# Kernel optimization log

Hardware: AMD Instinct MI355X
Metric: run time of the kernel (lower is better)

## Reference

```python
import jax, jax.numpy as jnp
import numpy as np

D_MODEL = 512
HEADS = 8

def setup_inputs() -> dict:
    key = jax.random.key(0)
    ks = jax.random.split(key, 11)
    B, S, D = 2, 4096, D_MODEL
    s = 1.0 / np.sqrt(D)
    inp = {
        'q': jax.random.normal(ks[0], (B, S, D), jnp.float32),
        'k': jax.random.normal(ks[1], (B, S, D), jnp.float32),
        'v': jax.random.normal(ks[2], (B, S, D), jnp.float32),
        'Wq': jax.random.normal(ks[3], (D, D), jnp.float32) * s,
        'bq': jnp.zeros((D,), jnp.float32),
        'Wk': jax.random.normal(ks[4], (D, D), jnp.float32) * s,
        'bk': jnp.zeros((D,), jnp.float32),
        'Wv': jax.random.normal(ks[5], (D, D), jnp.float32) * s,
        'bv': jnp.zeros((D,), jnp.float32),
        'Wo': jax.random.normal(ks[6], (D, D), jnp.float32) * s,
        'bo': jnp.zeros((D,), jnp.float32),
    }
    return inp

def _split_heads(x, h):
    B, S, D = x.shape
    return x.reshape(B, S, h, D // h).transpose(0, 2, 1, 3)  # [B,H,S,Dh]

def reference(q, k, v, Wq, bq, Wk, bk, Wv, bv, Wo, bo):
    # torch Linear: y = x @ W.T + b
    qh = _split_heads(q @ Wq.T + bq, HEADS)
    kh = _split_heads(k @ Wk.T + bk, HEADS)
    vh = _split_heads(v @ Wv.T + bv, HEADS)
    d_tensor = qh.shape[-1]
    scale = 1.0 / jnp.sqrt(jnp.asarray(d_tensor, qh.dtype))
    score = jnp.einsum('bhqd,bhkd->bhqk', qh, kh) * scale  # [B,H,S,S]
    attn = jax.nn.softmax(score, axis=-1)
    out = jnp.einsum('bhqk,bhkd->bhqd', attn, vh)
    B, H, S, Dh = out.shape
    out = out.transpose(0, 2, 1, 3).reshape(B, S, H * Dh)
    return out @ Wo.T + bo
```

## Files before the change

kernel.cpp:

```cpp
#include <hip/hip_runtime.h>

typedef short bf16x8 __attribute__((ext_vector_type(8)));
typedef float f32x2 __attribute__((ext_vector_type(2)));
typedef float f32x4 __attribute__((ext_vector_type(4)));
typedef float f32x16 __attribute__((ext_vector_type(16)));
typedef unsigned short ushort_t;
typedef unsigned short us8 __attribute__((ext_vector_type(8)));
typedef unsigned short us4 __attribute__((ext_vector_type(4)));
typedef unsigned int u32x4 __attribute__((ext_vector_type(4)));
typedef unsigned int uint2v __attribute__((ext_vector_type(2)));

#define MFMA16(a, b, c) __builtin_amdgcn_mfma_f32_16x16x32_bf16((a), (b), (c), 0, 0, 0)
#define MFMA32(a, b, c) __builtin_amdgcn_mfma_f32_32x32x16_bf16((a), (b), (c), 0, 0, 0)

template <int N> struct ic { static constexpr int value = N; };

static __device__ __forceinline__ ushort_t f2bf(float f) {
    unsigned int u = __builtin_bit_cast(unsigned int, f);
    u += 0x7FFFu + ((u >> 16) & 1u);
    return (ushort_t)(u >> 16);
}

static __device__ __forceinline__ unsigned cvtpk(float lo, float hi) {
    unsigned r;
    asm("v_cvt_pk_bf16_f32 %0, %1, %2" : "=v"(r) : "v"(lo), "v"(hi));
    return r;
}

static __device__ __forceinline__ void gload16(const void* g, void* l) {
    __builtin_amdgcn_global_load_lds(
        (const __attribute__((address_space(1))) unsigned int*)g,
        (__attribute__((address_space(3))) unsigned int*)l,
        16, 0, 0);
}

__global__ __launch_bounds__(256) void cvt_w(const float* __restrict__ W0,
                                             const float* __restrict__ W1,
                                             const float* __restrict__ W2,
                                             const float* __restrict__ W3,
                                             ushort_t* __restrict__ dst) {
    const float* src = (blockIdx.y == 0) ? W0 : (blockIdx.y == 1) ? W1
                     : (blockIdx.y == 2) ? W2 : W3;
    const int i = (blockIdx.x * 256 + threadIdx.x) * 8;
    float4 f0 = *(const float4*)(src + i);
    float4 f1 = *(const float4*)(src + i + 4);
    unsigned tw[4] = {cvtpk(f0.x, f0.y), cvtpk(f0.z, f0.w),
                      cvtpk(f1.x, f1.y), cvtpk(f1.z, f1.w)};
    *(u32x4*)(dst + (size_t)blockIdx.y * 262144 + i) = *(u32x4*)tw;
}

__global__ __launch_bounds__(256) void gemm_qkv(const float* __restrict__ qi,
                                                const float* __restrict__ ki,
                                                const float* __restrict__ vi,
                                                const ushort_t* __restrict__ Wball,
                                                const float* __restrict__ bq,
                                                const float* __restrict__ bk,
                                                const float* __restrict__ bv,
                                                ushort_t* __restrict__ Qh,
                                                ushort_t* __restrict__ Kh,
                                                ushort_t* __restrict__ Vt,
                                                float Cs) {
    constexpr int K = 512;
    __shared__ ushort_t As[64][72];
    __shared__ ushort_t Bs[64][72];

    const int which = blockIdx.y;
    const float*    Ap   = (which == 0) ? qi : (which == 1) ? ki : vi;
    const ushort_t* Wb   = Wball + (size_t)which * 262144;
    const float*    bias = (which == 0) ? bq : (which == 1) ? bk : bv;
    ushort_t*       outp = (which == 0) ? Qh : (which == 1) ? Kh : Vt;

    int bid = blockIdx.x;
    bid = (bid & 7) * 128 + (bid >> 3);
    const int bm = bid >> 3;
    const int bn = bid & 7;
    const int m0 = bm * 64, n0 = bn * 64;
    const int t    = threadIdx.x;
    const int lane = t & 63;
    const int wv   = t >> 6;
    const int wm   = wv >> 1, wn = wv & 1;
    const int lrow = t >> 2;
    const int lcol = (t & 3) * 16;

    const int l15 = lane & 15;
    const int l16 = lane >> 4;

    f32x4 acc[2][2] = {};

    const float*    apf = Ap + (size_t)(m0 + lrow) * K + lcol;
    const ushort_t* bpb = Wb + (size_t)(n0 + lrow) * K + lcol;

    us8 br0, br1;
    f32x4 af[4];

    af[0] = *(const f32x4*)apf;       af[1] = *(const f32x4*)(apf + 4);
    af[2] = *(const f32x4*)(apf + 8); af[3] = *(const f32x4*)(apf + 12);
    br0 = *(const us8*)bpb; br1 = *(const us8*)(bpb + 8);

#pragma unroll 1
    for (int kt = 0; kt < K / 64; ++kt) {
        __syncthreads();
        {
            unsigned tw[8];
#pragma unroll
            for (int i = 0; i < 4; ++i) {
                tw[2 * i]     = cvtpk(af[i][0], af[i][1]);
                tw[2 * i + 1] = cvtpk(af[i][2], af[i][3]);
            }
            *(u32x4*)&As[lrow][lcol]     = *(u32x4*)tw;
            *(u32x4*)&As[lrow][lcol + 8] = *(u32x4*)(tw + 4);
        }
        *(us8*)&Bs[lrow][lcol]     = br0;
        *(us8*)&Bs[lrow][lcol + 8] = br1;
        __syncthreads();

        if (kt < K / 64 - 1) {
            const int off = (kt + 1) * 64;
            const float* s = apf + off;
            af[0] = *(const f32x4*)s;       af[1] = *(const f32x4*)(s + 4);
            af[2] = *(const f32x4*)(s + 8); af[3] = *(const f32x4*)(s + 12);
            br0 = *(const us8*)(bpb + off); br1 = *(const us8*)(bpb + off + 8);
        }

#pragma unroll
        for (int kk = 0; kk < 2; ++kk) {
            bf16x8 a0 = *(const bf16x8*)&As[wm * 32 + l15][kk * 32 + l16 * 8];
            bf16x8 a1 = *(const bf16x8*)&As[wm * 32 + 16 + l15][kk * 32 + l16 * 8];
            bf16x8 b0 = *(const bf16x8*)&Bs[wn * 32 + l15][kk * 32 + l16 * 8];
            bf16x8 b1 = *(const bf16x8*)&Bs[wn * 32 + 16 + l15][kk * 32 + l16 * 8];
            acc[0][0] = MFMA16(a0, b0, acc[0][0]);
            acc[0][1] = MFMA16(a0, b1, acc[0][1]);
            acc[1][0] = MFMA16(a1, b0, acc[1][0]);
            acc[1][1] = MFMA16(a1, b1, acc[1][1]);
        }
    }

#pragma unroll
    for (int i = 0; i < 2; ++i)
#pragma unroll
        for (int j = 0; j < 2; ++j) {
            const int n  = n0 + wn * 32 + j * 16 + l15;
            const float bv_ = bias[n];
            const int h = n >> 6, d = n & 63;
            if (which == 2) {
                const int mbase = m0 + wm * 32 + i * 16 + l16 * 4;
                const int b = mbase >> 12, key = mbase & 4095;
                const int keyr = key & 63;
                const int ks = keyr >> 4, hc = (keyr >> 3) & 1, e0 = keyr & 7;
                const int db = d >> 5, dr = d & 31;
                ushort_t tmp[4];
#pragma unroll
                for (int v = 0; v < 4; ++v) tmp[v] = f2bf(acc[i][j][v] + bv_);
                *(us4*)(outp + (size_t)(b * 8 + h) * 262144 +
                        (size_t)(key >> 6) * 4096 +
                        db * 2048 + ks * 512 + (hc * 32 + dr) * 8 + e0) = *(us4*)tmp;
            } else if (which == 1) {
                const int jd = d >> 4, hc = (d >> 3) & 1, e = d & 7;
#pragma unroll
                for (int v = 0; v < 4; ++v) {
                    const int m = m0 + wm * 32 + i * 16 + l16 * 4 + v;
                    const int b = m >> 12, s = m & 4095;
                    const int r = s & 63, kb2 = r >> 5, kr = r & 31;
                    outp[(size_t)(b * 8 + h) * 262144 + (size_t)(s >> 6) * 4096 +
                         kb2 * 2048 + jd * 512 + (hc * 32 + kr) * 8 + e] =
                        f2bf(acc[i][j][v] + bv_);
                }
            } else {
#pragma unroll
                for (int v = 0; v < 4; ++v) {
                    const int m = m0 + wm * 32 + i * 16 + l16 * 4 + v;
                    const int b = m >> 12, s = m & 4095;
                    outp[(((size_t)(b * 8 + h)) * 4096 + s) * 64 + d] =
                        f2bf((acc[i][j][v] + bv_) * Cs);
                }
            }
        }
}

__global__ __launch_bounds__(256) void gemm_out(const ushort_t* __restrict__ Ap,
                                                const ushort_t* __restrict__ Wb,
                                                const float* __restrict__ bias,
                                                float* __restrict__ outp) {
    constexpr int K = 512;
    __shared__ ushort_t As[64][72];
    __shared__ ushort_t Bs[64][72];

    int bid = blockIdx.x;
    bid = (bid & 7) * 128 + (bid >> 3);
    const int bm = bid >> 3;
    const int bn = bid & 7;
    const int m0 = bm * 64, n0 = bn * 64;
    const int t    = threadIdx.x;
    const int lane = t & 63;
    const int wv   = t >> 6;
    const int wm   = wv >> 1, wn = wv & 1;
    const int lrow = t >> 2;
    const int lcol = (t & 3) * 16;

    const int l15 = lane & 15;
    const int l16 = lane >> 4;

    f32x4 acc[2][2] = {};

    const ushort_t* apb = Ap + (size_t)(m0 + lrow) * K + lcol;
    const ushort_t* bpb = Wb + (size_t)(n0 + lrow) * K + lcol;

    us8 ar0, ar1, br0, br1;
    ar0 = *(const us8*)apb; ar1 = *(const us8*)(apb + 8);
    br0 = *(const us8*)bpb; br1 = *(const us8*)(bpb + 8);

#pragma unroll 1
    for (int kt = 0; kt < K / 64; ++kt) {
        __syncthreads();
        *(us8*)&As[lrow][lcol]     = ar0;
        *(us8*)&As[lrow][lcol + 8] = ar1;
        *(us8*)&Bs[lrow][lcol]     = br0;
        *(us8*)&Bs[lrow][lcol + 8] = br1;
        __syncthreads();

        if (kt < K / 64 - 1) {
            const int off = (kt + 1) * 64;
            ar0 = *(const us8*)(apb + off); ar1 = *(const us8*)(apb + off + 8);
            br0 = *(const us8*)(bpb + off); br1 = *(const us8*)(bpb + off + 8);
        }

#pragma unroll
        for (int kk = 0; kk < 2; ++kk) {
            bf16x8 a0 = *(const bf16x8*)&As[wm * 32 + l15][kk * 32 + l16 * 8];
            bf16x8 a1 = *(const bf16x8*)&As[wm * 32 + 16 + l15][kk * 32 + l16 * 8];
            bf16x8 b0 = *(const bf16x8*)&Bs[wn * 32 + l15][kk * 32 + l16 * 8];
            bf16x8 b1 = *(const bf16x8*)&Bs[wn * 32 + 16 + l15][kk * 32 + l16 * 8];
            acc[0][0] = MFMA16(a0, b0, acc[0][0]);
            acc[0][1] = MFMA16(a0, b1, acc[0][1]);
            acc[1][0] = MFMA16(a1, b0, acc[1][0]);
            acc[1][1] = MFMA16(a1, b1, acc[1][1]);
        }
    }

#pragma unroll
    for (int i = 0; i < 2; ++i)
#pragma unroll
        for (int j = 0; j < 2; ++j) {
            const int n  = n0 + wn * 32 + j * 16 + l15;
            const float bv_ = bias[n];
#pragma unroll
            for (int v = 0; v < 4; ++v) {
                const int m = m0 + wm * 32 + i * 16 + l16 * 4 + v;
                outp[(size_t)m * 512 + n] = acc[i][j][v] + bv_;
            }
        }
}

__global__ __launch_bounds__(256) void attn_fwd(const ushort_t* __restrict__ Qh,
                                                const ushort_t* __restrict__ Kg,
                                                const ushort_t* __restrict__ Vg,
                                                ushort_t* __restrict__ Out) {
    constexpr int S  = 4096;
    constexpr int NT = 64;
    __shared__ __attribute__((aligned(16))) char LDS[32768];

    const int qt = blockIdx.x;
    const int bh = blockIdx.y;
    const int b  = bh >> 3, h = bh & 7;

    const int t    = threadIdx.x;
    const int lane = t & 63;
    const int wv   = t >> 6;
    const int l31  = lane & 31;
    const int hl   = lane >> 5;

    const int qw = qt * 128 + wv * 32;

    bf16x8 qf[4];
    {
        const ushort_t* qp = Qh + ((size_t)bh * S + qw + l31) * 64 + hl * 8;
#pragma unroll
        for (int ds = 0; ds < 4; ++ds) qf[ds] = *(const bf16x8*)(qp + ds * 16);
    }

    const f32x16 fzero = {};
    f32x16 accO[2] = {};
    float ll = 0.f;

    const char* lbase = LDS + lane * 16;
    const int wvb = wv * 1024;
    const ushort_t* kg = Kg + (size_t)bh * 262144 + wv * 512 + lane * 8;
    const ushort_t* vg = Vg + (size_t)bh * 262144 + wv * 512 + lane * 8;

    auto issue = [&](int kt, auto curc) {
        constexpr int CUR = decltype(curc)::value;
        const ushort_t* kg_ = kg + (size_t)kt * 4096;
        const ushort_t* vg_ = vg + (size_t)kt * 4096;
        gload16(kg_,        LDS + CUR * 8192 + wvb);
        gload16(kg_ + 2048, LDS + CUR * 8192 + 4096 + wvb);
        gload16(vg_,        LDS + 16384 + CUR * 8192 + wvb);
        gload16(vg_ + 2048, LDS + 16384 + CUR * 8192 + 4096 + wvb);
    };

    auto tile = [&](int kt, auto curc) {
        constexpr int CUR = decltype(curc)::value;

        f32x16 sc0, sc1;
        __builtin_amdgcn_s_setprio(1);
        {
            bf16x8 kf = *(const bf16x8*)(lbase + CUR * 8192);
            sc0 = MFMA32(kf, qf[0], fzero);
        }
#pragma unroll
        for (int ds = 1; ds < 4; ++ds) {
            bf16x8 kf = *(const bf16x8*)(lbase + CUR * 8192 + ds * 1024);
            sc0 = MFMA32(kf, qf[ds], sc0);
        }
        {
            bf16x8 kf = *(const bf16x8*)(lbase + CUR * 8192 + 4096);
            sc1 = MFMA32(kf, qf[0], fzero);
        }
#pragma unroll
        for (int ds = 1; ds < 4; ++ds) {
            bf16x8 kf = *(const bf16x8*)(lbase + CUR * 8192 + 4096 + ds * 1024);
            sc1 = MFMA32(kf, qf[ds], sc1);
        }
        __builtin_amdgcn_s_setprio(0);

#pragma unroll
        for (int i = 0; i < 16; ++i) {
            sc0[i] = __builtin_amdgcn_exp2f(sc0[i]);
            sc1[i] = __builtin_amdgcn_exp2f(sc1[i]);
        }

        {
#define PAIR(v, i) __builtin_shufflevector((v), (v), 2 * (i), 2 * (i) + 1)
            f32x2 pa = (PAIR(sc0, 0) + PAIR(sc0, 1)) + (PAIR(sc0, 2) + PAIR(sc0, 3));
            f32x2 pbt = (PAIR(sc0, 4) + PAIR(sc0, 5)) + (PAIR(sc0, 6) + PAIR(sc0, 7));
            f32x2 pc = (PAIR(sc1, 0) + PAIR(sc1, 1)) + (PAIR(sc1, 2) + PAIR(sc1, 3));
            f32x2 pd = (PAIR(sc1, 4) + PAIR(sc1, 5)) + (PAIR(sc1, 6) + PAIR(sc1, 7));
            f32x2 s2 = (pa + pbt) + (pc + pd);
            ll += s2.x + s2.y;
#undef PAIR
        }

        bf16x8 pb[4];
#pragma unroll
        for (int ks = 0; ks < 4; ++ks) {
            const int R0 = (ks & 1) * 8;
            float e0, e1, e2, e3, e4, e5, e6, e7;
            if (ks < 2) {
                e0 = sc0[R0+0]; e1 = sc0[R0+1]; e2 = sc0[R0+2]; e3 = sc0[R0+3];
                e4 = sc0[R0+4]; e5 = sc0[R0+5]; e6 = sc0[R0+6]; e7 = sc0[R0+7];
            } else {
                e0 = sc1[R0+0]; e1 = sc1[R0+1]; e2 = sc1[R0+2]; e3 = sc1[R0+3];
                e4 = sc1[R0+4]; e5 = sc1[R0+5]; e6 = sc1[R0+6]; e7 = sc1[R0+7];
            }
            unsigned w0 = cvtpk(e0, e1);
            unsigned w1 = cvtpk(e2, e3);
            unsigned w2 = cvtpk(e4, e5);
            unsigned w3 = cvtpk(e6, e7);
            uint2v s02 = __builtin_amdgcn_permlane32_swap(w0, w2, false, false);
            uint2v s13 = __builtin_amdgcn_permlane32_swap(w1, w3, false, false);
            u32x4 w = {s02.x, s13.x, s02.y, s13.y};
            pb[ks] = __builtin_bit_cast(bf16x8, w);
        }

        __builtin_amdgcn_s_setprio(1);
#pragma unroll
        for (int ks = 0; ks < 4; ++ks) {
            {
                bf16x8 vf = *(const bf16x8*)(lbase + 16384 + CUR * 8192 + ks * 1024);
                accO[0] = MFMA32(vf, pb[ks], accO[0]);
            }
            {
                bf16x8 vf = *(const bf16x8*)(lbase + 16384 + CUR * 8192 + 4096 + ks * 1024);
                accO[1] = MFMA32(vf, pb[ks], accO[1]);
            }
        }
        __builtin_amdgcn_s_setprio(0);

        __syncthreads();
        if (kt + 2 < NT) issue(kt + 2, curc);
    };

    issue(0, ic<0>{});
    issue(1, ic<1>{});
    __syncthreads();

#pragma unroll 1
    for (int kt2 = 0; kt2 < NT; kt2 += 2) {
        tile(kt2,     ic<0>{});
        tile(kt2 + 1, ic<1>{});
    }

    const float lt  = ll + __shfl_xor(ll, 32);
    const float inv = 1.0f / lt;
    ushort_t* orow = Out + ((size_t)b * S + qw + l31) * 512 + h * 64;
#pragma unroll
    for (int db = 0; db < 2; ++db)
#pragma unroll
        for (int q4 = 0; q4 < 4; ++q4) {
            unsigned w0 = cvtpk(accO[db][q4 * 4 + 0] * inv, accO[db][q4 * 4 + 1] * inv);
            unsigned w1 = cvtpk(accO[db][q4 * 4 + 2] * inv, accO[db][q4 * 4 + 3] * inv);
            unsigned tmp[2] = {w0, w1};
            *(us4*)(orow + db * 32 + q4 * 8 + hl * 4) = *(const us4*)tmp;
        }
}

extern "C" void kernel_launch(void* const* d_in, const int* in_sizes, int n_in,
                              void* d_out, int out_size, void* d_ws, size_t ws_size,
                              hipStream_t stream) {
    const float* q  = (const float*)d_in[0];
    const float* k  = (const float*)d_in[1];
    const float* v  = (const float*)d_in[2];
    const float* Wq = (const float*)d_in[3];
    const float* bq = (const float*)d_in[4];
    const float* bk = (const float*)d_in[6];
    const float* bv = (const float*)d_in[8];
    const float* bo = (const float*)d_in[10];

    char* w = (char*)d_ws;
    const size_t SZ = (size_t)2 * 8 * 4096 * 64 * 2;

    ushort_t* Qh  = (ushort_t*)(w);
    ushort_t* Kh  = (ushort_t*)(w + SZ);
    ushort_t* Vtr = (ushort_t*)(w + 2 * SZ);
    ushort_t* AO  = (ushort_t*)(w + 3 * SZ);
    ushort_t* Wb  = (ushort_t*)(w + 4 * SZ);

    cvt_w<<<dim3(128, 4), 256, 0, stream>>>(Wq, (const float*)d_in[5],
                                            (const float*)d_in[7], (const float*)d_in[9], Wb);

    const float Cs = 0.125f * 1.44269504f;
    gemm_qkv<<<dim3(1024, 3), 256, 0, stream>>>(q, k, v, Wb, bq, bk, bv, Qh, Kh, Vtr, Cs);

    attn_fwd<<<dim3(32, 16), 256, 0, stream>>>(Qh, Kh, Vtr, AO);

    gemm_out<<<1024, 256, 0, stream>>>(AO, Wb + 3 * 262144, bo, (float*)d_out);
}
```

Measured before the change: 140.4 us.

## Process two 32-row query groups per wave and remap blocks by XCD

```diff
diff --git a/kernel.cpp b/kernel.cpp
--- a/kernel.cpp
+++ b/kernel.cpp
@@ -259,9 +259,12 @@
     constexpr int NT = 64;
     __shared__ __attribute__((aligned(16))) char LDS[32768];
 
-    const int qt = blockIdx.x;
-    const int bh = blockIdx.y;
-    const int b  = bh >> 3, h = bh & 7;
+    const int id   = blockIdx.x;
+    const int xcd  = id & 7;
+    const int slot = id >> 3;
+    const int qt   = slot & 15;
+    const int bh   = xcd * 2 + (slot >> 4);
+    const int b    = bh >> 3, h = bh & 7;
 
     const int t    = threadIdx.x;
     const int lane = t & 63;
@@ -269,18 +272,19 @@
     const int l31  = lane & 31;
     const int hl   = lane >> 5;
 
-    const int qw = qt * 128 + wv * 32;
-
-    bf16x8 qf[4];
-    {
-        const ushort_t* qp = Qh + ((size_t)bh * S + qw + l31) * 64 + hl * 8;
-#pragma unroll
-        for (int ds = 0; ds < 4; ++ds) qf[ds] = *(const bf16x8*)(qp + ds * 16);
+    const int qw = qt * 256 + wv * 64;
+
+    bf16x8 qf[2][4];
+#pragma unroll
+    for (int g = 0; g < 2; ++g) {
+        const ushort_t* qp = Qh + ((size_t)bh * S + qw + g * 32 + l31) * 64 + hl * 8;
+#pragma unroll
+        for (int ds = 0; ds < 4; ++ds) qf[g][ds] = *(const bf16x8*)(qp + ds * 16);
     }
 
     const f32x16 fzero = {};
-    f32x16 accO[2] = {};
-    float ll = 0.f;
+    f32x16 accO[2][2] = {};
+    float ll[2] = {0.f, 0.f};
 
     const char* lbase = LDS + lane * 16;
     const int wvb = wv * 1024;
@@ -300,79 +304,69 @@
     auto tile = [&](int kt, auto curc) {
         constexpr int CUR = decltype(curc)::value;
 
-        f32x16 sc0, sc1;
+        f32x16 sc[2][2];
         __builtin_amdgcn_s_setprio(1);
-        {
-            bf16x8 kf = *(const bf16x8*)(lbase + CUR * 8192);
-            sc0 = MFMA32(kf, qf[0], fzero);
-        }
-#pragma unroll
-        for (int ds = 1; ds < 4; ++ds) {
-            bf16x8 kf = *(const bf16x8*)(lbase + CUR * 8192 + ds * 1024);
-            sc0 = MFMA32(kf, qf[ds], sc0);
-        }
-        {
-            bf16x8 kf = *(const bf16x8*)(lbase + CUR * 8192 + 4096);
-            sc1 = MFMA32(kf, qf[0], fzero);
-        }
-#pragma unroll
-        for (int ds = 1; ds < 4; ++ds) {
-            bf16x8 kf = *(const bf16x8*)(lbase + CUR * 8192 + 4096 + ds * 1024);
-            sc1 = MFMA32(kf, qf[ds], sc1);
+#pragma unroll
+        for (int kb = 0; kb < 2; ++kb) {
+            {
+                bf16x8 kf = *(const bf16x8*)(lbase + CUR * 8192 + kb * 4096);
+                sc[0][kb] = MFMA32(kf, qf[0][0], fzero);
+                sc[1][kb] = MFMA32(kf, qf[1][0], fzero);
+            }
+#pragma unroll
+            for (int ds = 1; ds < 4; ++ds) {
+                bf16x8 kf = *(const bf16x8*)(lbase + CUR * 8192 + kb * 4096 + ds * 1024);
+                sc[0][kb] = MFMA32(kf, qf[0][ds], sc[0][kb]);
+                sc[1][kb] = MFMA32(kf, qf[1][ds], sc[1][kb]);
+            }
         }
         __builtin_amdgcn_s_setprio(0);
 
 #pragma unroll
-        for (int i = 0; i < 16; ++i) {
-            sc0[i] = __builtin_amdgcn_exp2f(sc0[i]);
-            sc1[i] = __builtin_amdgcn_exp2f(sc1[i]);
-        }
-
-        {
+        for (int g = 0; g < 2; ++g)
+#pragma unroll
+            for (int kb = 0; kb < 2; ++kb)
+#pragma unroll
+                for (int i = 0; i < 16; ++i)
+                    sc[g][kb][i] = __builtin_amdgcn_exp2f(sc[g][kb][i]);
+
+#pragma unroll
+        for (int g = 0; g < 2; ++g) {
 #define PAIR(v, i) __builtin_shufflevector((v), (v), 2 * (i), 2 * (i) + 1)
-            f32x2 pa = (PAIR(sc0, 0) + PAIR(sc0, 1)) + (PAIR(sc0, 2) + PAIR(sc0, 3));
-            f32x2 pbt = (PAIR(sc0, 4) + PAIR(sc0, 5)) + (PAIR(sc0, 6) + PAIR(sc0, 7));
-            f32x2 pc = (PAIR(sc1, 0) + PAIR(sc1, 1)) + (PAIR(sc1, 2) + PAIR(sc1, 3));
-            f32x2 pd = (PAIR(sc1, 4) + PAIR(sc1, 5)) + (PAIR(sc1, 6) + PAIR(sc1, 7));
-            f32x2 s2 = (pa + pbt) + (pc + pd);
-            ll += s2.x + s2.y;
+            f32x2 pa  = (PAIR(sc[g][0], 0) + PAIR(sc[g][0], 1)) + (PAIR(sc[g][0], 2) + PAIR(sc[g][0], 3));
+            f32x2 pbt = (PAIR(sc[g][0], 4) + PAIR(sc[g][0], 5)) + (PAIR(sc[g][0], 6) + PAIR(sc[g][0], 7));
+            f32x2 pc  = (PAIR(sc[g][1], 0) + PAIR(sc[g][1], 1)) + (PAIR(sc[g][1], 2) + PAIR(sc[g][1], 3));
+            f32x2 pd  = (PAIR(sc[g][1], 4) + PAIR(sc[g][1], 5)) + (PAIR(sc[g][1], 6) + PAIR(sc[g][1], 7));
+            f32x2 s2  = (pa + pbt) + (pc + pd);
+            ll[g] += s2.x + s2.y;
 #undef PAIR
         }
 
-        bf16x8 pb[4];
-#pragma unroll
-        for (int ks = 0; ks < 4; ++ks) {
-            const int R0 = (ks & 1) * 8;
-            float e0, e1, e2, e3, e4, e5, e6, e7;
-            if (ks < 2) {
-                e0 = sc0[R0+0]; e1 = sc0[R0+1]; e2 = sc0[R0+2]; e3 = sc0[R0+3];
-                e4 = sc0[R0+4]; e5 = sc0[R0+5]; e6 = sc0[R0+6]; e7 = sc0[R0+7];
-            } else {
-                e0 = sc1[R0+0]; e1 = sc1[R0+1]; e2 = sc1[R0+2]; e3 = sc1[R0+3];
-                e4 = sc1[R0+4]; e5 = sc1[R0+5]; e6 = sc1[R0+6]; e7 = sc1[R0+7];
-            }
-            unsigned w0 = cvtpk(e0, e1);
-            unsigned w1 = cvtpk(e2, e3);
-            unsigned w2 = cvtpk(e4, e5);
-            unsigned w3 = cvtpk(e6, e7);
-            uint2v s02 = __builtin_amdgcn_permlane32_swap(w0, w2, false, false);
-            uint2v s13 = __builtin_amdgcn_permlane32_swap(w1, w3, false, false);
-            u32x4 w = {s02.x, s13.x, s02.y, s13.y};
-            pb[ks] = __builtin_bit_cast(bf16x8, w);
-        }
+        bf16x8 pb[2][4];
+#pragma unroll
+        for (int g = 0; g < 2; ++g)
+#pragma unroll
+            for (int ks = 0; ks < 4; ++ks) {
+                const int kb = ks >> 1, R0 = (ks & 1) * 8;
+                unsigned w0 = cvtpk(sc[g][kb][R0 + 0], sc[g][kb][R0 + 1]);
+                unsigned w1 = cvtpk(sc[g][kb][R0 + 2], sc[g][kb][R0 + 3]);
+                unsigned w2 = cvtpk(sc[g][kb][R0 + 4], sc[g][kb][R0 + 5]);
+                unsigned w3 = cvtpk(sc[g][kb][R0 + 6], sc[g][kb][R0 + 7]);
+                uint2v s02 = __builtin_amdgcn_permlane32_swap(w0, w2, false, false);
+                uint2v s13 = __builtin_amdgcn_permlane32_swap(w1, w3, false, false);
+                u32x4 w = {s02.x, s13.x, s02.y, s13.y};
+                pb[g][ks] = __builtin_bit_cast(bf16x8, w);
+            }
 
         __builtin_amdgcn_s_setprio(1);
 #pragma unroll
-        for (int ks = 0; ks < 4; ++ks) {
-            {
-                bf16x8 vf = *(const bf16x8*)(lbase + 16384 + CUR * 8192 + ks * 1024);
-                accO[0] = MFMA32(vf, pb[ks], accO[0]);
-            }
-            {
-                bf16x8 vf = *(const bf16x8*)(lbase + 16384 + CUR * 8192 + 4096 + ks * 1024);
-                accO[1] = MFMA32(vf, pb[ks], accO[1]);
-            }
-        }
+        for (int ks = 0; ks < 4; ++ks)
+#pragma unroll
+            for (int db = 0; db < 2; ++db) {
+                bf16x8 vf = *(const bf16x8*)(lbase + 16384 + CUR * 8192 + db * 4096 + ks * 1024);
+                accO[0][db] = MFMA32(vf, pb[0][ks], accO[0][db]);
+                accO[1][db] = MFMA32(vf, pb[1][ks], accO[1][db]);
+            }
         __builtin_amdgcn_s_setprio(0);
 
         __syncthreads();
@@ -389,18 +383,21 @@
         tile(kt2 + 1, ic<1>{});
     }
 
-    const float lt  = ll + __shfl_xor(ll, 32);
-    const float inv = 1.0f / lt;
-    ushort_t* orow = Out + ((size_t)b * S + qw + l31) * 512 + h * 64;
-#pragma unroll
-    for (int db = 0; db < 2; ++db)
-#pragma unroll
-        for (int q4 = 0; q4 < 4; ++q4) {
-            unsigned w0 = cvtpk(accO[db][q4 * 4 + 0] * inv, accO[db][q4 * 4 + 1] * inv);
-            unsigned w1 = cvtpk(accO[db][q4 * 4 + 2] * inv, accO[db][q4 * 4 + 3] * inv);
-            unsigned tmp[2] = {w0, w1};
-            *(us4*)(orow + db * 32 + q4 * 8 + hl * 4) = *(const us4*)tmp;
-        }
+#pragma unroll
+    for (int g = 0; g < 2; ++g) {
+        const float lt  = ll[g] + __shfl_xor(ll[g], 32);
+        const float inv = 1.0f / lt;
+        ushort_t* orow = Out + ((size_t)b * S + qw + g * 32 + l31) * 512 + h * 64;
+#pragma unroll
+        for (int db = 0; db < 2; ++db)
+#pragma unroll
+            for (int q4 = 0; q4 < 4; ++q4) {
+                unsigned w0 = cvtpk(accO[g][db][q4 * 4 + 0] * inv, accO[g][db][q4 * 4 + 1] * inv);
+                unsigned w1 = cvtpk(accO[g][db][q4 * 4 + 2] * inv, accO[g][db][q4 * 4 + 3] * inv);
+                unsigned tmp[2] = {w0, w1};
+                *(us4*)(orow + db * 32 + q4 * 8 + hl * 4) = *(const us4*)tmp;
+            }
+    }
 }
 
 extern "C" void kernel_launch(void* const* d_in, const int* in_sizes, int n_in,
@@ -430,7 +427,7 @@
     const float Cs = 0.125f * 1.44269504f;
     gemm_qkv<<<dim3(1024, 3), 256, 0, stream>>>(q, k, v, Wb, bq, bk, bv, Qh, Kh, Vtr, Cs);
 
-    attn_fwd<<<dim3(32, 16), 256, 0, stream>>>(Qh, Kh, Vtr, AO);
+    attn_fwd<<<256, 256, 0, stream>>>(Qh, Kh, Vtr, AO);
 
     gemm_out<<<1024, 256, 0, stream>>>(AO, Wb + 3 * 262144, bo, (float*)d_out);
 }
```

Result: slower. 144.6 us (+2.9%).

## Fuse weight conversion into GEMMs, double attention KV tile, remap blocks per XCD

Applied to the files above, without the earlier changes.

```diff
diff --git a/kernel.cpp b/kernel.cpp
--- a/kernel.cpp
+++ b/kernel.cpp
@@ -34,25 +34,12 @@
         16, 0, 0);
 }
 
-__global__ __launch_bounds__(256) void cvt_w(const float* __restrict__ W0,
-                                             const float* __restrict__ W1,
-                                             const float* __restrict__ W2,
-                                             const float* __restrict__ W3,
-                                             ushort_t* __restrict__ dst) {
-    const float* src = (blockIdx.y == 0) ? W0 : (blockIdx.y == 1) ? W1
-                     : (blockIdx.y == 2) ? W2 : W3;
-    const int i = (blockIdx.x * 256 + threadIdx.x) * 8;
-    float4 f0 = *(const float4*)(src + i);
-    float4 f1 = *(const float4*)(src + i + 4);
-    unsigned tw[4] = {cvtpk(f0.x, f0.y), cvtpk(f0.z, f0.w),
-                      cvtpk(f1.x, f1.y), cvtpk(f1.z, f1.w)};
-    *(u32x4*)(dst + (size_t)blockIdx.y * 262144 + i) = *(u32x4*)tw;
-}
-
 __global__ __launch_bounds__(256) void gemm_qkv(const float* __restrict__ qi,
                                                 const float* __restrict__ ki,
                                                 const float* __restrict__ vi,
-                                                const ushort_t* __restrict__ Wball,
+                                                const float* __restrict__ Wq,
+                                                const float* __restrict__ Wk,
+                                                const float* __restrict__ Wv,
                                                 const float* __restrict__ bq,
                                                 const float* __restrict__ bk,
                                                 const float* __restrict__ bv,
@@ -65,10 +52,10 @@
     __shared__ ushort_t Bs[64][72];
 
     const int which = blockIdx.y;
-    const float*    Ap   = (which == 0) ? qi : (which == 1) ? ki : vi;
-    const ushort_t* Wb   = Wball + (size_t)which * 262144;
-    const float*    bias = (which == 0) ? bq : (which == 1) ? bk : bv;
-    ushort_t*       outp = (which == 0) ? Qh : (which == 1) ? Kh : Vt;
+    const float* Ap   = (which == 0) ? qi : (which == 1) ? ki : vi;
+    const float* Wf   = (which == 0) ? Wq : (which == 1) ? Wk : Wv;
+    const float* bias = (which == 0) ? bq : (which == 1) ? bk : bv;
+    ushort_t*    outp = (which == 0) ? Qh : (which == 1) ? Kh : Vt;
 
     int bid = blockIdx.x;
     bid = (bid & 7) * 128 + (bid >> 3);
@@ -87,15 +74,14 @@
 
     f32x4 acc[2][2] = {};
 
-    const float*    apf = Ap + (size_t)(m0 + lrow) * K + lcol;
-    const ushort_t* bpb = Wb + (size_t)(n0 + lrow) * K + lcol;
-
-    us8 br0, br1;
-    f32x4 af[4];
-
-    af[0] = *(const f32x4*)apf;       af[1] = *(const f32x4*)(apf + 4);
-    af[2] = *(const f32x4*)(apf + 8); af[3] = *(const f32x4*)(apf + 12);
-    br0 = *(const us8*)bpb; br1 = *(const us8*)(bpb + 8);
+    const float* apf = Ap + (size_t)(m0 + lrow) * K + lcol;
+    const float* bpf = Wf + (size_t)(n0 + lrow) * K + lcol;
+
+    f32x4 af[4], bfr[4];
+    af[0] = *(const f32x4*)apf;        af[1] = *(const f32x4*)(apf + 4);
+    af[2] = *(const f32x4*)(apf + 8);  af[3] = *(const f32x4*)(apf + 12);
+    bfr[0] = *(const f32x4*)bpf;       bfr[1] = *(const f32x4*)(bpf + 4);
+    bfr[2] = *(const f32x4*)(bpf + 8); bfr[3] = *(const f32x4*)(bpf + 12);
 
 #pragma unroll 1
     for (int kt = 0; kt < K / 64; ++kt) {
@@ -109,17 +95,25 @@
             }
             *(u32x4*)&As[lrow][lcol]     = *(u32x4*)tw;
             *(u32x4*)&As[lrow][lcol + 8] = *(u32x4*)(tw + 4);
-        }
-        *(us8*)&Bs[lrow][lcol]     = br0;
-        *(us8*)&Bs[lrow][lcol + 8] = br1;
+            unsigned tb[8];
+#pragma unroll
+            for (int i = 0; i < 4; ++i) {
+                tb[2 * i]     = cvtpk(bfr[i][0], bfr[i][1]);
+                tb[2 * i + 1] = cvtpk(bfr[i][2], bfr[i][3]);
+            }
+            *(u32x4*)&Bs[lrow][lcol]     = *(u32x4*)tb;
+            *(u32x4*)&Bs[lrow][lcol + 8] = *(u32x4*)(tb + 4);
+        }
         __syncthreads();
 
         if (kt < K / 64 - 1) {
             const int off = (kt + 1) * 64;
-            const float* s = apf + off;
-            af[0] = *(const f32x4*)s;       af[1] = *(const f32x4*)(s + 4);
-            af[2] = *(const f32x4*)(s + 8); af[3] = *(const f32x4*)(s + 12);
-            br0 = *(const us8*)(bpb + off); br1 = *(const us8*)(bpb + off + 8);
+            const float* s  = apf + off;
+            const float* sb = bpf + off;
+            af[0] = *(const f32x4*)s;        af[1] = *(const f32x4*)(s + 4);
+            af[2] = *(const f32x4*)(s + 8);  af[3] = *(const f32x4*)(s + 12);
+            bfr[0] = *(const f32x4*)sb;      bfr[1] = *(const f32x4*)(sb + 4);
+            bfr[2] = *(const f32x4*)(sb + 8); bfr[3] = *(const f32x4*)(sb + 12);
         }
 
 #pragma unroll
@@ -178,7 +172,7 @@
 }
 
 __global__ __launch_bounds__(256) void gemm_out(const ushort_t* __restrict__ Ap,
-                                                const ushort_t* __restrict__ Wb,
+                                                const float* __restrict__ Wf,
                                                 const float* __restrict__ bias,
                                                 float* __restrict__ outp) {
     constexpr int K = 512;
@@ -203,25 +197,37 @@
     f32x4 acc[2][2] = {};
 
     const ushort_t* apb = Ap + (size_t)(m0 + lrow) * K + lcol;
-    const ushort_t* bpb = Wb + (size_t)(n0 + lrow) * K + lcol;
-
-    us8 ar0, ar1, br0, br1;
+    const float*    bpf = Wf + (size_t)(n0 + lrow) * K + lcol;
+
+    us8 ar0, ar1;
+    f32x4 bfr[4];
     ar0 = *(const us8*)apb; ar1 = *(const us8*)(apb + 8);
-    br0 = *(const us8*)bpb; br1 = *(const us8*)(bpb + 8);
+    bfr[0] = *(const f32x4*)bpf;       bfr[1] = *(const f32x4*)(bpf + 4);
+    bfr[2] = *(const f32x4*)(bpf + 8); bfr[3] = *(const f32x4*)(bpf + 12);
 
 #pragma unroll 1
     for (int kt = 0; kt < K / 64; ++kt) {
         __syncthreads();
         *(us8*)&As[lrow][lcol]     = ar0;
         *(us8*)&As[lrow][lcol + 8] = ar1;
-        *(us8*)&Bs[lrow][lcol]     = br0;
-        *(us8*)&Bs[lrow][lcol + 8] = br1;
+        {
+            unsigned tb[8];
+#pragma unroll
+            for (int i = 0; i < 4; ++i) {
+                tb[2 * i]     = cvtpk(bfr[i][0], bfr[i][1]);
+                tb[2 * i + 1] = cvtpk(bfr[i][2], bfr[i][3]);
+            }
+            *(u32x4*)&Bs[lrow][lcol]     = *(u32x4*)tb;
+            *(u32x4*)&Bs[lrow][lcol + 8] = *(u32x4*)(tb + 4);
+        }
         __syncthreads();
 
         if (kt < K / 64 - 1) {
             const int off = (kt + 1) * 64;
             ar0 = *(const us8*)(apb + off); ar1 = *(const us8*)(apb + off + 8);
-            br0 = *(const us8*)(bpb + off); br1 = *(const us8*)(bpb + off + 8);
+            const float* sb = bpf + off;
+            bfr[0] = *(const f32x4*)sb;       bfr[1] = *(const f32x4*)(sb + 4);
+            bfr[2] = *(const f32x4*)(sb + 8); bfr[3] = *(const f32x4*)(sb + 12);
         }
 
 #pragma unroll
@@ -256,12 +262,15 @@
                                                 const ushort_t* __restrict__ Vg,
                                                 ushort_t* __restrict__ Out) {
     constexpr int S  = 4096;
-    constexpr int NT = 64;
-    __shared__ __attribute__((aligned(16))) char LDS[32768];
-
-    const int qt = blockIdx.x;
-    const int bh = blockIdx.y;
-    const int b  = bh >> 3, h = bh & 7;
+    constexpr int NT = 32;
+    __shared__ __attribute__((aligned(16))) char LDS[65536];
+
+    const int id   = blockIdx.x;
+    const int xcd  = id & 7;
+    const int slot = id >> 3;
+    const int qt   = slot & 31;
+    const int bh   = xcd * 2 + (slot >> 5);
+    const int b    = bh >> 3, h = bh & 7;
 
     const int t    = threadIdx.x;
     const int lane = t & 63;
@@ -289,35 +298,40 @@
 
     auto issue = [&](int kt, auto curc) {
         constexpr int CUR = decltype(curc)::value;
-        const ushort_t* kg_ = kg + (size_t)kt * 4096;
-        const ushort_t* vg_ = vg + (size_t)kt * 4096;
-        gload16(kg_,        LDS + CUR * 8192 + wvb);
-        gload16(kg_ + 2048, LDS + CUR * 8192 + 4096 + wvb);
-        gload16(vg_,        LDS + 16384 + CUR * 8192 + wvb);
-        gload16(vg_ + 2048, LDS + 16384 + CUR * 8192 + 4096 + wvb);
+        const ushort_t* kg_ = kg + (size_t)kt * 8192;
+        const ushort_t* vg_ = vg + (size_t)kt * 8192;
+#pragma unroll
+        for (int c = 0; c < 4; ++c)
+            gload16(kg_ + c * 2048, LDS + CUR * 16384 + c * 4096 + wvb);
+#pragma unroll
+        for (int c = 0; c < 4; ++c)
+            gload16(vg_ + c * 2048, LDS + 32768 + CUR * 16384 + c * 4096 + wvb);
     };
 
-    auto tile = [&](int kt, auto curc) {
+    auto sub = [&](auto curc, auto sc_) {
         constexpr int CUR = decltype(curc)::value;
+        constexpr int SB  = decltype(sc_)::value;
+        constexpr int KB  = CUR * 16384 + SB * 8192;
+        constexpr int VB  = 32768 + CUR * 16384 + SB * 8192;
 
         f32x16 sc0, sc1;
         __builtin_amdgcn_s_setprio(1);
         {
-            bf16x8 kf = *(const bf16x8*)(lbase + CUR * 8192);
+            bf16x8 kf = *(const bf16x8*)(lbase + KB);
             sc0 = MFMA32(kf, qf[0], fzero);
         }
 #pragma unroll
         for (int ds = 1; ds < 4; ++ds) {
-            bf16x8 kf = *(const bf16x8*)(lbase + CUR * 8192 + ds * 1024);
+            bf16x8 kf = *(const bf16x8*)(lbase + KB + ds * 1024);
             sc0 = MFMA32(kf, qf[ds], sc0);
         }
         {
-            bf16x8 kf = *(const bf16x8*)(lbase + CUR * 8192 + 4096);
+            bf16x8 kf = *(const bf16x8*)(lbase + KB + 4096);
             sc1 = MFMA32(kf, qf[0], fzero);
         }
 #pragma unroll
         for (int ds = 1; ds < 4; ++ds) {
-            bf16x8 kf = *(const bf16x8*)(lbase + CUR * 8192 + 4096 + ds * 1024);
+            bf16x8 kf = *(const bf16x8*)(lbase + KB + 4096 + ds * 1024);
             sc1 = MFMA32(kf, qf[ds], sc1);
         }
         __builtin_amdgcn_s_setprio(0);
@@ -330,11 +344,11 @@
 
         {
 #define PAIR(v, i) __builtin_shufflevector((v), (v), 2 * (i), 2 * (i) + 1)
-            f32x2 pa = (PAIR(sc0, 0) + PAIR(sc0, 1)) + (PAIR(sc0, 2) + PAIR(sc0, 3));
+            f32x2 pa  = (PAIR(sc0, 0) + PAIR(sc0, 1)) + (PAIR(sc0, 2) + PAIR(sc0, 3));
             f32x2 pbt = (PAIR(sc0, 4) + PAIR(sc0, 5)) + (PAIR(sc0, 6) + PAIR(sc0, 7));
-            f32x2 pc = (PAIR(sc1, 0) + PAIR(sc1, 1)) + (PAIR(sc1, 2) + PAIR(sc1, 3));
-            f32x2 pd = (PAIR(sc1, 4) + PAIR(sc1, 5)) + (PAIR(sc1, 6) + PAIR(sc1, 7));
-            f32x2 s2 = (pa + pbt) + (pc + pd);
+            f32x2 pc  = (PAIR(sc1, 0) + PAIR(sc1, 1)) + (PAIR(sc1, 2) + PAIR(sc1, 3));
+            f32x2 pd  = (PAIR(sc1, 4) + PAIR(sc1, 5)) + (PAIR(sc1, 6) + PAIR(sc1, 7));
+            f32x2 s2  = (pa + pbt) + (pc + pd);
             ll += s2.x + s2.y;
 #undef PAIR
         }
@@ -365,16 +379,20 @@
 #pragma unroll
         for (int ks = 0; ks < 4; ++ks) {
             {
-                bf16x8 vf = *(const bf16x8*)(lbase + 16384 + CUR * 8192 + ks * 1024);
+                bf16x8 vf = *(const bf16x8*)(lbase + VB + ks * 1024);
                 accO[0] = MFMA32(vf, pb[ks], accO[0]);
             }
             {
-                bf16x8 vf = *(const bf16x8*)(lbase + 16384 + CUR * 8192 + 4096 + ks * 1024);
+                bf16x8 vf = *(const bf16x8*)(lbase + VB + 4096 + ks * 1024);
                 accO[1] = MFMA32(vf, pb[ks], accO[1]);
             }
         }
         __builtin_amdgcn_s_setprio(0);
-
+    };
+
+    auto tile = [&](int kt, auto curc) {
+        sub(curc, ic<0>{});
+        sub(curc, ic<1>{});
         __syncthreads();
         if (kt + 2 < NT) issue(kt + 2, curc);
     };
@@ -411,8 +429,11 @@
     const float* v  = (const float*)d_in[2];
     const float* Wq = (const float*)d_in[3];
     const float* bq = (const float*)d_in[4];
+    const float* Wk = (const float*)d_in[5];
     const float* bk = (const float*)d_in[6];
+    const float* Wv = (const float*)d_in[7];
     const float* bv = (const float*)d_in[8];
+    const float* Wo = (const float*)d_in[9];
     const float* bo = (const float*)d_in[10];
 
     char* w = (char*)d_ws;
@@ -422,15 +443,12 @@
     ushort_t* Kh  = (ushort_t*)(w + SZ);
     ushort_t* Vtr = (ushort_t*)(w + 2 * SZ);
     ushort_t* AO  = (ushort_t*)(w + 3 * SZ);
-    ushort_t* Wb  = (ushort_t*)(w + 4 * SZ);
-
-    cvt_w<<<dim3(128, 4), 256, 0, stream>>>(Wq, (const float*)d_in[5],
-                                            (const float*)d_in[7], (const float*)d_in[9], Wb);
 
     const float Cs = 0.125f * 1.44269504f;
-    gemm_qkv<<<dim3(1024, 3), 256, 0, stream>>>(q, k, v, Wb, bq, bk, bv, Qh, Kh, Vtr, Cs);
-
-    attn_fwd<<<dim3(32, 16), 256, 0, stream>>>(Qh, Kh, Vtr, AO);
-
-    gemm_out<<<1024, 256, 0, stream>>>(AO, Wb + 3 * 262144, bo, (float*)d_out);
-}
+    gemm_qkv<<<dim3(1024, 3), 256, 0, stream>>>(q, k, v, Wq, Wk, Wv, bq, bk, bv,
+                                                Qh, Kh, Vtr, Cs);
+
+    attn_fwd<<<512, 256, 0, stream>>>(Qh, Kh, Vtr, AO);
+
+    gemm_out<<<1024, 256, 0, stream>>>(AO, Wo, bo, (float*)d_out);
+}
```

New measurement: 169.5 us. 20.7% more time.

## Software-pipeline QK of next tile with softmax/PV and remap blocks per XCD

Applied to the files above, without the earlier changes.

```diff
diff --git a/kernel.cpp b/kernel.cpp
--- a/kernel.cpp
+++ b/kernel.cpp
@@ -256,12 +256,14 @@
                                                 const ushort_t* __restrict__ Vg,
                                                 ushort_t* __restrict__ Out) {
     constexpr int S  = 4096;
-    constexpr int NT = 64;
-    __shared__ __attribute__((aligned(16))) char LDS[32768];
-
-    const int qt = blockIdx.x;
-    const int bh = blockIdx.y;
-    const int b  = bh >> 3, h = bh & 7;
+    __shared__ __attribute__((aligned(16))) char LDS[40960];
+
+    const int id   = blockIdx.x;
+    const int xcd  = id & 7;
+    const int slot = id >> 3;
+    const int qt   = slot & 31;
+    const int bh   = xcd * 2 + (slot >> 5);
+    const int b    = bh >> 3, h = bh & 7;
 
     const int t    = threadIdx.x;
     const int lane = t & 63;
@@ -287,58 +289,57 @@
     const ushort_t* kg = Kg + (size_t)bh * 262144 + wv * 512 + lane * 8;
     const ushort_t* vg = Vg + (size_t)bh * 262144 + wv * 512 + lane * 8;
 
-    auto issue = [&](int kt, auto curc) {
-        constexpr int CUR = decltype(curc)::value;
-        const ushort_t* kg_ = kg + (size_t)kt * 4096;
-        const ushort_t* vg_ = vg + (size_t)kt * 4096;
-        gload16(kg_,        LDS + CUR * 8192 + wvb);
-        gload16(kg_ + 2048, LDS + CUR * 8192 + 4096 + wvb);
-        gload16(vg_,        LDS + 16384 + CUR * 8192 + wvb);
-        gload16(vg_ + 2048, LDS + 16384 + CUR * 8192 + 4096 + wvb);
+    auto issueK = [&](int kt, int kslotB) {
+        const ushort_t* p = kg + (size_t)kt * 4096;
+        gload16(p,        LDS + kslotB + wvb);
+        gload16(p + 2048, LDS + kslotB + 4096 + wvb);
     };
-
-    auto tile = [&](int kt, auto curc) {
-        constexpr int CUR = decltype(curc)::value;
-
-        f32x16 sc0, sc1;
+    auto issueV = [&](int kt, int vslotB) {
+        const ushort_t* p = vg + (size_t)kt * 4096;
+        gload16(p,        LDS + vslotB + wvb);
+        gload16(p + 2048, LDS + vslotB + 4096 + wvb);
+    };
+
+    auto QK = [&](auto kc, f32x16& s0, f32x16& s1) {
+        constexpr int KB = decltype(kc)::value;
         __builtin_amdgcn_s_setprio(1);
         {
-            bf16x8 kf = *(const bf16x8*)(lbase + CUR * 8192);
-            sc0 = MFMA32(kf, qf[0], fzero);
+            bf16x8 kf = *(const bf16x8*)(lbase + KB);
+            s0 = MFMA32(kf, qf[0], fzero);
         }
 #pragma unroll
         for (int ds = 1; ds < 4; ++ds) {
-            bf16x8 kf = *(const bf16x8*)(lbase + CUR * 8192 + ds * 1024);
-            sc0 = MFMA32(kf, qf[ds], sc0);
+            bf16x8 kf = *(const bf16x8*)(lbase + KB + ds * 1024);
+            s0 = MFMA32(kf, qf[ds], s0);
         }
         {
-            bf16x8 kf = *(const bf16x8*)(lbase + CUR * 8192 + 4096);
-            sc1 = MFMA32(kf, qf[0], fzero);
+            bf16x8 kf = *(const bf16x8*)(lbase + KB + 4096);
+            s1 = MFMA32(kf, qf[0], fzero);
         }
 #pragma unroll
         for (int ds = 1; ds < 4; ++ds) {
-            bf16x8 kf = *(const bf16x8*)(lbase + CUR * 8192 + 4096 + ds * 1024);
-            sc1 = MFMA32(kf, qf[ds], sc1);
+            bf16x8 kf = *(const bf16x8*)(lbase + KB + 4096 + ds * 1024);
+            s1 = MFMA32(kf, qf[ds], s1);
         }
         __builtin_amdgcn_s_setprio(0);
-
+    };
+
+    auto SOFTPV = [&](f32x16& sc0, f32x16& sc1, int vbase) {
 #pragma unroll
         for (int i = 0; i < 16; ++i) {
             sc0[i] = __builtin_amdgcn_exp2f(sc0[i]);
             sc1[i] = __builtin_amdgcn_exp2f(sc1[i]);
         }
-
         {
 #define PAIR(v, i) __builtin_shufflevector((v), (v), 2 * (i), 2 * (i) + 1)
-            f32x2 pa = (PAIR(sc0, 0) + PAIR(sc0, 1)) + (PAIR(sc0, 2) + PAIR(sc0, 3));
+            f32x2 pa  = (PAIR(sc0, 0) + PAIR(sc0, 1)) + (PAIR(sc0, 2) + PAIR(sc0, 3));
             f32x2 pbt = (PAIR(sc0, 4) + PAIR(sc0, 5)) + (PAIR(sc0, 6) + PAIR(sc0, 7));
-            f32x2 pc = (PAIR(sc1, 0) + PAIR(sc1, 1)) + (PAIR(sc1, 2) + PAIR(sc1, 3));
-            f32x2 pd = (PAIR(sc1, 4) + PAIR(sc1, 5)) + (PAIR(sc1, 6) + PAIR(sc1, 7));
-            f32x2 s2 = (pa + pbt) + (pc + pd);
+            f32x2 pc  = (PAIR(sc1, 0) + PAIR(sc1, 1)) + (PAIR(sc1, 2) + PAIR(sc1, 3));
+            f32x2 pd  = (PAIR(sc1, 4) + PAIR(sc1, 5)) + (PAIR(sc1, 6) + PAIR(sc1, 7));
+            f32x2 s2  = (pa + pbt) + (pc + pd);
             ll += s2.x + s2.y;
 #undef PAIR
         }
-
         bf16x8 pb[4];
 #pragma unroll
         for (int ks = 0; ks < 4; ++ks) {
@@ -360,34 +361,56 @@
             u32x4 w = {s02.x, s13.x, s02.y, s13.y};
             pb[ks] = __builtin_bit_cast(bf16x8, w);
         }
-
+        const char* vb = LDS + vbase + lane * 16;
         __builtin_amdgcn_s_setprio(1);
 #pragma unroll
         for (int ks = 0; ks < 4; ++ks) {
             {
-                bf16x8 vf = *(const bf16x8*)(lbase + 16384 + CUR * 8192 + ks * 1024);
+                bf16x8 vf = *(const bf16x8*)(vb + ks * 1024);
                 accO[0] = MFMA32(vf, pb[ks], accO[0]);
             }
             {
-                bf16x8 vf = *(const bf16x8*)(lbase + 16384 + CUR * 8192 + 4096 + ks * 1024);
+                bf16x8 vf = *(const bf16x8*)(vb + 4096 + ks * 1024);
                 accO[1] = MFMA32(vf, pb[ks], accO[1]);
             }
         }
         __builtin_amdgcn_s_setprio(0);
-
-        __syncthreads();
-        if (kt + 2 < NT) issue(kt + 2, curc);
     };
 
-    issue(0, ic<0>{});
-    issue(1, ic<1>{});
+    int v0b = 16384, v1b = 24576, v2b = 32768;
+
+    issueK(0, 0);
+    issueK(1, 8192);
+    issueV(0, v0b);
+    issueV(1, v1b);
     __syncthreads();
 
+    f32x16 sA0, sA1, sB0, sB1;
+    QK(ic<0>{}, sA0, sA1);
+
 #pragma unroll 1
-    for (int kt2 = 0; kt2 < NT; kt2 += 2) {
-        tile(kt2,     ic<0>{});
-        tile(kt2 + 1, ic<1>{});
+    for (int tp = 0; tp < 31; ++tp) {
+        const int te = 2 * tp;
+        __syncthreads();
+        issueK(te + 2, 0);
+        issueV(te + 2, v2b);
+        QK(ic<8192>{}, sB0, sB1);
+        SOFTPV(sA0, sA1, v0b);
+        { int tmp = v0b; v0b = v1b; v1b = v2b; v2b = tmp; }
+        __syncthreads();
+        issueK(te + 3, 8192);
+        issueV(te + 3, v2b);
+        QK(ic<0>{}, sA0, sA1);
+        SOFTPV(sB0, sB1, v0b);
+        { int tmp = v0b; v0b = v1b; v1b = v2b; v2b = tmp; }
     }
+
+    __syncthreads();
+    QK(ic<8192>{}, sB0, sB1);
+    SOFTPV(sA0, sA1, v0b);
+    { int tmp = v0b; v0b = v1b; v1b = v2b; v2b = tmp; }
+
+    SOFTPV(sB0, sB1, v0b);
 
     const float lt  = ll + __shfl_xor(ll, 32);
     const float inv = 1.0f / lt;
@@ -430,7 +453,7 @@
     const float Cs = 0.125f * 1.44269504f;
     gemm_qkv<<<dim3(1024, 3), 256, 0, stream>>>(q, k, v, Wb, bq, bk, bv, Qh, Kh, Vtr, Cs);
 
-    attn_fwd<<<dim3(32, 16), 256, 0, stream>>>(Qh, Kh, Vtr, AO);
+    attn_fwd<<<512, 256, 0, stream>>>(Qh, Kh, Vtr, AO);
 
     gemm_out<<<1024, 256, 0, stream>>>(AO, Wb + 3 * 262144, bo, (float*)d_out);
 }
```

Measured after the change: 136.8 us. 2.6% less time.
